# Performance work log

Hardware: AMD Instinct MI355X
Metric: run time of the kernel (lower is better)

Reference implementation:

```python
import jax, jax.numpy as jnp
import numpy as np

N_GRID = 262144   # grid vertices (all local, empty halo)
N_MESH = 40962    # icosahedral mesh level-6 vertices
N_EDGES = 524288  # mesh2grid bipartite edges
H = 128           # cfg.model.hidden_dim
LN_EPS = 1e-5


def layer_norm(x, g, b):
    m = jnp.mean(x, axis=-1, keepdims=True)
    v = jnp.var(x, axis=-1, keepdims=True)
    return (x - m) * jax.lax.rsqrt(v + LN_EPS) * g + b


def setup_inputs() -> dict:
    key = jax.random.key(0)
    ks = jax.random.split(key, 12)
    def w(k, shape, fan_in):
        return jax.random.normal(k, shape, jnp.float32) * (fan_in ** -0.5)
    return {
        "mesh2grid_edge_features": jax.random.normal(ks[0], (N_EDGES, H), jnp.float32),
        "grid_node_features": jax.random.normal(ks[1], (N_GRID, H), jnp.float32),
        "mesh_node_features": jax.random.normal(ks[2], (N_MESH, H), jnp.float32),
        # edge MLP: Linear(3H->H) -> SiLU -> Linear(H->H) -> LayerNorm, residual
        "edge_W1": w(ks[3], (3 * H, H), 3 * H), "edge_b1": jnp.zeros((H,), jnp.float32),
        "edge_W2": w(ks[4], (H, H), H), "edge_b2": jnp.zeros((H,), jnp.float32),
        "edge_ln_g": jnp.ones((H,), jnp.float32), "edge_ln_b": jnp.zeros((H,), jnp.float32),
        # node MLP: Linear(2H->H) -> SiLU -> Linear(H->H) -> LayerNorm
        "node_W1": w(ks[5], (2 * H, H), 2 * H), "node_b1": jnp.zeros((H,), jnp.float32),
        "node_W2": w(ks[6], (H, H), H), "node_b2": jnp.zeros((H,), jnp.float32),
        "node_ln_g": jnp.ones((H,), jnp.float32), "node_ln_b": jnp.zeros((H,), jnp.float32),
        "src_indices": jax.random.randint(ks[7], (N_EDGES,), 0, N_MESH, jnp.int32),
        "dst_indices": jax.random.randint(ks[8], (N_EDGES,), 0, N_GRID, jnp.int32),
    }


def reference(mesh2grid_edge_features, grid_node_features, mesh_node_features,
              edge_W1, edge_b1, edge_W2, edge_b2, edge_ln_g, edge_ln_b,
              node_W1, node_b1, node_W2, node_b2, node_ln_g, node_ln_b,
              src_indices, dst_indices):
    # --- edge block: gather src (mesh) / dst (grid), MLP, LN, residual ---
    src = mesh_node_features[src_indices]        # [E, H]  (augmented mesh == mesh, empty halo)
    dst = grid_node_features[dst_indices]        # [E, H]
    xe = jnp.concatenate([src, dst, mesh2grid_edge_features], axis=-1)  # [E, 3H]
    he = (jax.nn.silu(xe @ edge_W1 + edge_b1)) @ edge_W2 + edge_b2
    e_feats = mesh2grid_edge_features + layer_norm(he, edge_ln_g, edge_ln_b)  # [E, H]
    # --- node block: scatter-sum edges to grid nodes, MLP, LN ---
    agg = jax.ops.segment_sum(e_feats, dst_indices, num_segments=N_GRID)  # [N_grid, H]
    xn = jnp.concatenate([grid_node_features, agg], axis=-1)              # [N_grid, 2H]
    hn = (jax.nn.silu(xn @ node_W1 + node_b1)) @ node_W2 + node_b2
    n_feats = layer_norm(hn, node_ln_g, node_ln_b)
    return grid_node_features + n_feats
```

## Files before the change

kernel.cpp:

```cpp
#include <hip/hip_runtime.h>
#include <stdint.h>

#define HDIM 128
#define NGRID 262144
#define NMESH 40962
#define NEDGE 524288

typedef __attribute__((ext_vector_type(8))) short short8;
typedef __attribute__((ext_vector_type(4))) float f32x4;

__device__ __forceinline__ unsigned short f2bf(float f) {
  union { float f; uint32_t u; } v; v.f = f;
  uint32_t u = v.u;
  u += 0x7fffu + ((u >> 16) & 1u);
  return (unsigned short)(u >> 16);
}
__device__ __forceinline__ float bf2f(unsigned short h) {
  union { uint32_t u; float f; } v; v.u = ((uint32_t)h) << 16;
  return v.f;
}
__device__ __forceinline__ short8 cvt8(float4 a, float4 b) {
  short8 r;
  r[0] = (short)f2bf(a.x); r[1] = (short)f2bf(a.y);
  r[2] = (short)f2bf(a.z); r[3] = (short)f2bf(a.w);
  r[4] = (short)f2bf(b.x); r[5] = (short)f2bf(b.y);
  r[6] = (short)f2bf(b.z); r[7] = (short)f2bf(b.w);
  return r;
}

__global__ void pack_weights(const float* __restrict__ eW1, const float* __restrict__ eW2,
                             const float* __restrict__ nW1, const float* __restrict__ nW2,
                             unsigned short* __restrict__ ws)
{
  int i = blockIdx.x * 256 + threadIdx.x;
  unsigned short* eW1T = ws;
  unsigned short* eW2T = ws + 49152;
  unsigned short* nW1T = ws + 65536;
  unsigned short* nW2T = ws + 98304;
  if (i < 49152) {
    int c = i / 384, k = i % 384;
    eW1T[i] = f2bf(eW1[(size_t)k * 128 + c]);
  } else if (i < 65536) {
    int j = i - 49152; int c = j / 128, k = j % 128;
    eW2T[j] = f2bf(eW2[(size_t)k * 128 + c]);
  } else if (i < 98304) {
    int j = i - 65536; int c = j / 256, k = j % 256;
    nW1T[j] = f2bf(nW1[(size_t)k * 128 + c]);
  } else if (i < 114688) {
    int j = i - 98304; int c = j / 128, k = j % 128;
    nW2T[j] = f2bf(nW2[(size_t)k * 128 + c]);
  }
}

__global__ __launch_bounds__(256, 4)
void edge_kernel(const float* __restrict__ ef, const float* __restrict__ gridf,
                 const float* __restrict__ mesh,
                 const unsigned short* __restrict__ W1T, const unsigned short* __restrict__ W2T,
                 const float* __restrict__ b1, const float* __restrict__ b2,
                 const float* __restrict__ lng, const float* __restrict__ lnb,
                 const int* __restrict__ src, const int* __restrict__ dst,
                 float* __restrict__ agg)
{
  __shared__ __align__(16) unsigned short h1s[64][136];

  const int tid  = threadIdx.x;
  const int wave = tid >> 6;
  const int lane = tid & 63;
  const int l16  = lane & 15;
  const int g4   = lane >> 4;
  const int e0   = blockIdx.x * 64;
  const int arow = wave * 16 + l16;

  const int myS = src[e0 + arow];
  const int myD = dst[e0 + arow];
  const float* rowS = mesh  + (size_t)myS * HDIM;
  const float* rowD = gridf + (size_t)myD * HDIM;
  const float* rowE = ef    + (size_t)(e0 + arow) * HDIM;

  f32x4 acc[8];
  #pragma unroll
  for (int c = 0; c < 8; ++c) acc[c] = (f32x4){0.f, 0.f, 0.f, 0.f};

  const unsigned short* wl1 = W1T + (size_t)l16 * 384 + g4 * 8;

  #pragma unroll
  for (int part = 0; part < 3; ++part) {
    const float* base = (part == 0) ? rowS : (part == 1) ? rowD : rowE;
    #pragma unroll
    for (int kk = 0; kk < 4; ++kk) {
      const int ks = part * 4 + kk;
      const float* ap = base + kk * 32 + g4 * 8;
      float4 f0 = *reinterpret_cast<const float4*>(ap);
      float4 f1 = *reinterpret_cast<const float4*>(ap + 4);
      short8 a = cvt8(f0, f1);
      #pragma unroll
      for (int c = 0; c < 8; ++c) {
        short8 b = *reinterpret_cast<const short8*>(wl1 + (size_t)c * 16 * 384 + ks * 32);
        acc[c] = __builtin_amdgcn_mfma_f32_16x16x32_bf16(a, b, acc[c], 0, 0, 0);
      }
    }
  }

  #pragma unroll
  for (int c = 0; c < 8; ++c) {
    const int col = c * 16 + l16;
    float bb = b1[col];
    #pragma unroll
    for (int r = 0; r < 4; ++r) {
      float x = acc[c][r] + bb;
      float s = x / (1.f + __expf(-x));
      unsigned int h = f2bf(s);
      unsigned int other = __shfl_xor((int)h, 1);
      unsigned int packed = (l16 & 1) ? ((h << 16) | other) : ((other << 16) | h);
      if ((l16 & 1) == (r & 1)) {
        *reinterpret_cast<unsigned int*>(&h1s[wave * 16 + g4 * 4 + r][c * 16 + (l16 & ~1)]) = packed;
      }
    }
  }
  __syncthreads();

  f32x4 acc2[8];
  #pragma unroll
  for (int c = 0; c < 8; ++c) acc2[c] = (f32x4){0.f, 0.f, 0.f, 0.f};

  const unsigned short* wl2 = W2T + (size_t)l16 * 128 + g4 * 8;
  #pragma unroll
  for (int ks = 0; ks < 4; ++ks) {
    short8 a = *reinterpret_cast<const short8*>(&h1s[arow][ks * 32 + g4 * 8]);
    #pragma unroll
    for (int c = 0; c < 8; ++c) {
      short8 b = *reinterpret_cast<const short8*>(wl2 + (size_t)c * 16 * 128 + ks * 32);
      acc2[c] = __builtin_amdgcn_mfma_f32_16x16x32_bf16(a, b, acc2[c], 0, 0, 0);
    }
  }

  float vs[4] = {0.f, 0.f, 0.f, 0.f};
  float vq[4] = {0.f, 0.f, 0.f, 0.f};
  #pragma unroll
  for (int c = 0; c < 8; ++c) {
    float bb = b2[c * 16 + l16];
    #pragma unroll
    for (int r = 0; r < 4; ++r) {
      float x = acc2[c][r] + bb;
      acc2[c][r] = x;
      vs[r] += x;
      vq[r] += x * x;
    }
  }
  #pragma unroll
  for (int m = 1; m < 16; m <<= 1) {
    #pragma unroll
    for (int r = 0; r < 4; ++r) {
      vs[r] += __shfl_xor(vs[r], m);
      vq[r] += __shfl_xor(vq[r], m);
    }
  }
  float mean[4], rstd[4];
  #pragma unroll
  for (int r = 0; r < 4; ++r) {
    mean[r] = vs[r] * (1.f / 128.f);
    float var = vq[r] * (1.f / 128.f) - mean[r] * mean[r];
    rstd[r] = rsqrtf(var + 1e-5f);
  }
  int drow[4];
  #pragma unroll
  for (int r = 0; r < 4; ++r) drow[r] = dst[e0 + wave * 16 + g4 * 4 + r];

  #pragma unroll
  for (int c = 0; c < 8; ++c) {
    const int col = c * 16 + l16;
    float gg = lng[col], bb = lnb[col];
    #pragma unroll
    for (int r = 0; r < 4; ++r) {
      const int row = wave * 16 + g4 * 4 + r;
      float y = (acc2[c][r] - mean[r]) * rstd[r] * gg + bb;
      float e = ef[(size_t)(e0 + row) * HDIM + col] + y;
      unsafeAtomicAdd(&agg[(size_t)drow[r] * HDIM + col], e);
    }
  }
}

__global__ __launch_bounds__(256, 4)
void node_kernel(const float* __restrict__ gridf,
                 const unsigned short* __restrict__ W1T, const unsigned short* __restrict__ W2T,
                 const float* __restrict__ b1, const float* __restrict__ b2,
                 const float* __restrict__ lng, const float* __restrict__ lnb,
                 float* __restrict__ out)
{
  __shared__ __align__(16) unsigned short h1s[64][136];

  const int tid  = threadIdx.x;
  const int wave = tid >> 6;
  const int lane = tid & 63;
  const int l16  = lane & 15;
  const int g4   = lane >> 4;
  const int n0   = blockIdx.x * 64;
  const int arow = wave * 16 + l16;

  const float* rowG = gridf + (size_t)(n0 + arow) * HDIM;
  const float* rowA = out   + (size_t)(n0 + arow) * HDIM;

  f32x4 acc[8];
  #pragma unroll
  for (int c = 0; c < 8; ++c) acc[c] = (f32x4){0.f, 0.f, 0.f, 0.f};

  const unsigned short* wl1 = W1T + (size_t)l16 * 256 + g4 * 8;

  #pragma unroll
  for (int part = 0; part < 2; ++part) {
    const float* base = (part == 0) ? rowG : rowA;
    #pragma unroll
    for (int kk = 0; kk < 4; ++kk) {
      const int ks = part * 4 + kk;
      const float* ap = base + kk * 32 + g4 * 8;
      float4 f0 = *reinterpret_cast<const float4*>(ap);
      float4 f1 = *reinterpret_cast<const float4*>(ap + 4);
      short8 a = cvt8(f0, f1);
      #pragma unroll
      for (int c = 0; c < 8; ++c) {
        short8 b = *reinterpret_cast<const short8*>(wl1 + (size_t)c * 16 * 256 + ks * 32);
        acc[c] = __builtin_amdgcn_mfma_f32_16x16x32_bf16(a, b, acc[c], 0, 0, 0);
      }
    }
  }

  #pragma unroll
  for (int c = 0; c < 8; ++c) {
    const int col = c * 16 + l16;
    float bb = b1[col];
    #pragma unroll
    for (int r = 0; r < 4; ++r) {
      float x = acc[c][r] + bb;
      float s = x / (1.f + __expf(-x));
      unsigned int h = f2bf(s);
      unsigned int other = __shfl_xor((int)h, 1);
      unsigned int packed = (l16 & 1) ? ((h << 16) | other) : ((other << 16) | h);
      if ((l16 & 1) == (r & 1)) {
        *reinterpret_cast<unsigned int*>(&h1s[wave * 16 + g4 * 4 + r][c * 16 + (l16 & ~1)]) = packed;
      }
    }
  }
  __syncthreads();

  f32x4 acc2[8];
  #pragma unroll
  for (int c = 0; c < 8; ++c) acc2[c] = (f32x4){0.f, 0.f, 0.f, 0.f};

  const unsigned short* wl2 = W2T + (size_t)l16 * 128 + g4 * 8;
  #pragma unroll
  for (int ks = 0; ks < 4; ++ks) {
    short8 a = *reinterpret_cast<const short8*>(&h1s[arow][ks * 32 + g4 * 8]);
    #pragma unroll
    for (int c = 0; c < 8; ++c) {
      short8 b = *reinterpret_cast<const short8*>(wl2 + (size_t)c * 16 * 128 + ks * 32);
      acc2[c] = __builtin_amdgcn_mfma_f32_16x16x32_bf16(a, b, acc2[c], 0, 0, 0);
    }
  }

  float vs[4] = {0.f, 0.f, 0.f, 0.f};
  float vq[4] = {0.f, 0.f, 0.f, 0.f};
  #pragma unroll
  for (int c = 0; c < 8; ++c) {
    float bb = b2[c * 16 + l16];
    #pragma unroll
    for (int r = 0; r < 4; ++r) {
      float x = acc2[c][r] + bb;
      acc2[c][r] = x;
      vs[r] += x;
      vq[r] += x * x;
    }
  }
  #pragma unroll
  for (int m = 1; m < 16; m <<= 1) {
    #pragma unroll
    for (int r = 0; r < 4; ++r) {
      vs[r] += __shfl_xor(vs[r], m);
      vq[r] += __shfl_xor(vq[r], m);
    }
  }
  float mean[4], rstd[4];
  #pragma unroll
  for (int r = 0; r < 4; ++r) {
    mean[r] = vs[r] * (1.f / 128.f);
    float var = vq[r] * (1.f / 128.f) - mean[r] * mean[r];
    rstd[r] = rsqrtf(var + 1e-5f);
  }
  #pragma unroll
  for (int c = 0; c < 8; ++c) {
    const int col = c * 16 + l16;
    float gg = lng[col], bb = lnb[col];
    #pragma unroll
    for (int r = 0; r < 4; ++r) {
      const int row = wave * 16 + g4 * 4 + r;
      size_t idx = (size_t)(n0 + row) * HDIM + col;
      float y = (acc2[c][r] - mean[r]) * rstd[r] * gg + bb;
      out[idx] = gridf[idx] + y;
    }
  }
}

extern "C" void kernel_launch(void* const* d_in, const int* in_sizes, int n_in,
                              void* d_out, int out_size, void* d_ws, size_t ws_size,
                              hipStream_t stream)
{
  (void)in_sizes; (void)n_in; (void)out_size; (void)ws_size;
  const float* ef   = (const float*)d_in[0];
  const float* grid = (const float*)d_in[1];
  const float* mesh = (const float*)d_in[2];
  const float* eW1  = (const float*)d_in[3];
  const float* eb1  = (const float*)d_in[4];
  const float* eW2  = (const float*)d_in[5];
  const float* eb2  = (const float*)d_in[6];
  const float* elng = (const float*)d_in[7];
  const float* elnb = (const float*)d_in[8];
  const float* nW1  = (const float*)d_in[9];
  const float* nb1  = (const float*)d_in[10];
  const float* nW2  = (const float*)d_in[11];
  const float* nb2  = (const float*)d_in[12];
  const float* nlng = (const float*)d_in[13];
  const float* nlnb = (const float*)d_in[14];
  const int* src    = (const int*)d_in[15];
  const int* dst    = (const int*)d_in[16];
  float* out = (float*)d_out;
  unsigned short* ws = (unsigned short*)d_ws;

  hipMemsetAsync(out, 0, (size_t)NGRID * HDIM * sizeof(float), stream);
  pack_weights<<<448, 256, 0, stream>>>(eW1, eW2, nW1, nW2, ws);
  edge_kernel<<<NEDGE / 64, 256, 0, stream>>>(ef, grid, mesh,
      ws, ws + 49152, eb1, eb2, elng, elnb, src, dst, out);
  node_kernel<<<NGRID / 64, 256, 0, stream>>>(grid,
      ws + 65536, ws + 98304, nb1, nb2, nlng, nlnb, out);
}
```

Baseline: 957.4 us.

## Sort edges by destination and fuse edge and node MLPs per grid tile

Builds a CSR of edges grouped by destination grid node using a histogram, a three-pass scan and a scatter. A single fused kernel then processes 32 grid nodes per block: it gathers their edges, runs the edge MLP with 32x32x16 MFMAs, accumulates into LDS with shared atomics, and runs the node MLP directly. This removes the global float atomics and the round trip of the aggregate through HBM, and swaps the MFMA shape and the weight fragment layout. In exchange it adds several small preprocessing launches, global atomics in the histogram and scatter, and uneven per-block work because the number of edges per node varies.

```diff
diff --git a/kernel.cpp b/kernel.cpp
--- a/kernel.cpp
+++ b/kernel.cpp
@@ -7,295 +7,287 @@
 #define NEDGE 524288
 
 typedef __attribute__((ext_vector_type(8))) short short8;
-typedef __attribute__((ext_vector_type(4))) float f32x4;
-
-__device__ __forceinline__ unsigned short f2bf(float f) {
-  union { float f; uint32_t u; } v; v.f = f;
-  uint32_t u = v.u;
+typedef __attribute__((ext_vector_type(16))) float f32x16;
+typedef unsigned int u32;
+typedef unsigned long long u64;
+
+#define WS_COUNT   0x000000u
+#define WS_ROWPTR  0x100000u
+#define WS_WLOC    0x200010u
+#define WS_BSUM    0x300100u
+#define WS_SORTED  0x310000u
+#define WS_WEIGHTS 0x800000u
+#define WE1 0u
+#define WE2 49152u
+#define WN1 65536u
+#define WN2 98304u
+
+static __device__ __forceinline__ u32 f2bf_u(float f) {
+  union { float f; u32 u; } v; v.f = f;
+  u32 u = v.u;
   u += 0x7fffu + ((u >> 16) & 1u);
-  return (unsigned short)(u >> 16);
-}
-__device__ __forceinline__ float bf2f(unsigned short h) {
-  union { uint32_t u; float f; } v; v.u = ((uint32_t)h) << 16;
-  return v.f;
-}
-__device__ __forceinline__ short8 cvt8(float4 a, float4 b) {
+  return u >> 16;
+}
+static __device__ __forceinline__ unsigned short f2bf(float f) { return (unsigned short)f2bf_u(f); }
+static __device__ __forceinline__ u32 pack2bf(float a, float b) {
+  return f2bf_u(a) | (f2bf_u(b) << 16);
+}
+static __device__ __forceinline__ short8 cvt8(const float* p) {
+  float4 f0 = *(const float4*)p;
+  float4 f1 = *(const float4*)(p + 4);
   short8 r;
-  r[0] = (short)f2bf(a.x); r[1] = (short)f2bf(a.y);
-  r[2] = (short)f2bf(a.z); r[3] = (short)f2bf(a.w);
-  r[4] = (short)f2bf(b.x); r[5] = (short)f2bf(b.y);
-  r[6] = (short)f2bf(b.z); r[7] = (short)f2bf(b.w);
+  r[0] = (short)f2bf_u(f0.x); r[1] = (short)f2bf_u(f0.y);
+  r[2] = (short)f2bf_u(f0.z); r[3] = (short)f2bf_u(f0.w);
+  r[4] = (short)f2bf_u(f1.x); r[5] = (short)f2bf_u(f1.y);
+  r[6] = (short)f2bf_u(f1.z); r[7] = (short)f2bf_u(f1.w);
   return r;
 }
 
 __global__ void pack_weights(const float* __restrict__ eW1, const float* __restrict__ eW2,
                              const float* __restrict__ nW1, const float* __restrict__ nW2,
-                             unsigned short* __restrict__ ws)
+                             unsigned short* __restrict__ wp)
 {
   int i = blockIdx.x * 256 + threadIdx.x;
-  unsigned short* eW1T = ws;
-  unsigned short* eW2T = ws + 49152;
-  unsigned short* nW1T = ws + 65536;
-  unsigned short* nW2T = ws + 98304;
-  if (i < 49152) {
-    int c = i / 384, k = i % 384;
-    eW1T[i] = f2bf(eW1[(size_t)k * 128 + c]);
-  } else if (i < 65536) {
-    int j = i - 49152; int c = j / 128, k = j % 128;
-    eW2T[j] = f2bf(eW2[(size_t)k * 128 + c]);
-  } else if (i < 98304) {
-    int j = i - 65536; int c = j / 256, k = j % 256;
-    nW1T[j] = f2bf(nW1[(size_t)k * 128 + c]);
-  } else if (i < 114688) {
-    int j = i - 98304; int c = j / 128, k = j % 128;
-    nW2T[j] = f2bf(nW2[(size_t)k * 128 + c]);
-  }
-}
-
-__global__ __launch_bounds__(256, 4)
-void edge_kernel(const float* __restrict__ ef, const float* __restrict__ gridf,
-                 const float* __restrict__ mesh,
-                 const unsigned short* __restrict__ W1T, const unsigned short* __restrict__ W2T,
-                 const float* __restrict__ b1, const float* __restrict__ b2,
-                 const float* __restrict__ lng, const float* __restrict__ lnb,
-                 const int* __restrict__ src, const int* __restrict__ dst,
-                 float* __restrict__ agg)
+  const float* W; int KS; u32 base; int j;
+  if (i < 49152)       { W = eW1; KS = 24; base = WE1; j = i; }
+  else if (i < 65536)  { W = eW2; KS = 8;  base = WE2; j = i - 49152; }
+  else if (i < 98304)  { W = nW1; KS = 16; base = WN1; j = i - 65536; }
+  else if (i < 114688) { W = nW2; KS = 8;  base = WN2; j = i - 98304; }
+  else return;
+  int ii = j & 7, l = (j >> 3) & 63, frag = j >> 9;
+  int ks = frag % KS, w = frag / KS;
+  int row = w * 32 + (l & 31);
+  int k = ks * 16 + (l >> 5) * 8 + ii;
+  wp[base + j] = f2bf(W[(size_t)k * 128 + row]);
+}
+
+__global__ void hist_k(const int* __restrict__ dst, u32* __restrict__ cnt) {
+  int e = blockIdx.x * 256 + threadIdx.x;
+  atomicAdd(&cnt[dst[e]], 1u);
+}
+
+__global__ void scan1(const u32* __restrict__ cnt, u32* __restrict__ rp, u32* __restrict__ bsum) {
+  int t = threadIdx.x, b = blockIdx.x;
+  int i0 = b * 1024 + t * 4;
+  uint4 v = *(const uint4*)(cnt + i0);
+  u32 s = v.x + v.y + v.z + v.w;
+  u32 sc = s;
+  #pragma unroll
+  for (int d = 1; d < 64; d <<= 1) {
+    u32 n = (u32)__shfl_up((int)sc, d);
+    if ((t & 63) >= d) sc += n;
+  }
+  __shared__ u32 wsum[4];
+  if ((t & 63) == 63) wsum[t >> 6] = sc;
+  __syncthreads();
+  u32 woff = 0;
+  for (int w = 0; w < (t >> 6); ++w) woff += wsum[w];
+  u32 ex = woff + sc - s;
+  rp[i0] = ex; rp[i0 + 1] = ex + v.x; rp[i0 + 2] = ex + v.x + v.y; rp[i0 + 3] = ex + v.x + v.y + v.z;
+  if (t == 255) bsum[b] = woff + sc;
+}
+
+__global__ void scan2(u32* __restrict__ bsum) {
+  int t = threadIdx.x;
+  u32 s = bsum[t];
+  u32 sc = s;
+  #pragma unroll
+  for (int d = 1; d < 64; d <<= 1) {
+    u32 n = (u32)__shfl_up((int)sc, d);
+    if ((t & 63) >= d) sc += n;
+  }
+  __shared__ u32 wsum[4];
+  if ((t & 63) == 63) wsum[t >> 6] = sc;
+  __syncthreads();
+  u32 woff = 0;
+  for (int w = 0; w < (t >> 6); ++w) woff += wsum[w];
+  bsum[t] = woff + sc - s;
+}
+
+__global__ void scan3(u32* __restrict__ rp, u32* __restrict__ wloc, const u32* __restrict__ bsum) {
+  int t = threadIdx.x, b = blockIdx.x;
+  int i0 = b * 1024 + t * 4;
+  u32 off = bsum[b];
+  #pragma unroll
+  for (int j = 0; j < 4; ++j) { u32 vv = rp[i0 + j] + off; rp[i0 + j] = vv; wloc[i0 + j] = vv; }
+  if (b == 0 && t == 0) rp[NGRID] = NEDGE;
+}
+
+__global__ void scatter_k(const int* __restrict__ src, const int* __restrict__ dst,
+                          u32* __restrict__ wloc, u64* __restrict__ sorted) {
+  int e = blockIdx.x * 256 + threadIdx.x;
+  int d = dst[e];
+  u32 pos = atomicAdd(&wloc[d], 1u);
+  sorted[pos] = (u64)(u32)src[e] | ((u64)(u32)d << 16) | ((u64)(u32)e << 34);
+}
+
+__global__ __launch_bounds__(256, 3)
+void fused_kernel(const float* __restrict__ ef, const float* __restrict__ gridf,
+                  const float* __restrict__ mesh,
+                  const unsigned short* __restrict__ wp,
+                  const float* __restrict__ eb1, const float* __restrict__ eb2,
+                  const float* __restrict__ elng, const float* __restrict__ elnb,
+                  const float* __restrict__ nb1, const float* __restrict__ nb2,
+                  const float* __restrict__ nlng, const float* __restrict__ nlnb,
+                  const u32* __restrict__ rowptr, const u64* __restrict__ sorted,
+                  float* __restrict__ out)
 {
-  __shared__ __align__(16) unsigned short h1s[64][136];
-
-  const int tid  = threadIdx.x;
-  const int wave = tid >> 6;
-  const int lane = tid & 63;
-  const int l16  = lane & 15;
-  const int g4   = lane >> 4;
-  const int e0   = blockIdx.x * 64;
-  const int arow = wave * 16 + l16;
-
-  const int myS = src[e0 + arow];
-  const int myD = dst[e0 + arow];
-  const float* rowS = mesh  + (size_t)myS * HDIM;
-  const float* rowD = gridf + (size_t)myD * HDIM;
-  const float* rowE = ef    + (size_t)(e0 + arow) * HDIM;
-
-  f32x4 acc[8];
-  #pragma unroll
-  for (int c = 0; c < 8; ++c) acc[c] = (f32x4){0.f, 0.f, 0.f, 0.f};
-
-  const unsigned short* wl1 = W1T + (size_t)l16 * 384 + g4 * 8;
-
-  #pragma unroll
-  for (int part = 0; part < 3; ++part) {
-    const float* base = (part == 0) ? rowS : (part == 1) ? rowD : rowE;
-    #pragma unroll
-    for (int kk = 0; kk < 4; ++kk) {
-      const int ks = part * 4 + kk;
-      const float* ap = base + kk * 32 + g4 * 8;
-      float4 f0 = *reinterpret_cast<const float4*>(ap);
-      float4 f1 = *reinterpret_cast<const float4*>(ap + 4);
-      short8 a = cvt8(f0, f1);
+  __shared__ unsigned short xeLDS[32 * 384];
+  __shared__ unsigned short h1LDS[32 * 128];
+  __shared__ float aggLDS[32 * 129];
+  __shared__ float statsLDS[4][32][2];
+  __shared__ u32 srE[32], dlE[32], oeE[32];
+
+  const int tid = threadIdx.x;
+  const int wv = tid >> 6, ln = tid & 63, l31 = ln & 63 & 31, hi = ln >> 5;
+  const int n0 = blockIdx.x * 32;
+  const int rs = (int)rowptr[n0], re = (int)rowptr[n0 + 32];
+  const int swzE = (l31 & 15) << 3;
+
+  for (int i = tid; i < 32 * 129; i += 256) aggLDS[i] = 0.f;
+  __syncthreads();
+
+  const short8* w1p = (const short8*)(wp + WE1) + wv * 24 * 64 + ln;
+  const short8* w2p = (const short8*)(wp + WE2) + wv * 8 * 64 + ln;
+
+  for (int base = rs; base < re; base += 32) {
+    if (tid < 32) {
+      int p = base + tid; if (p >= re) p = re - 1;
+      u64 v = sorted[p];
+      srE[tid] = (u32)(v & 0xffffu);
+      dlE[tid] = (u32)((v >> 16) & 0x3ffffu) - (u32)n0;
+      oeE[tid] = (u32)(v >> 34);
+    }
+    __syncthreads();
+    for (int j = tid; j < 32 * 48; j += 256) {
+      int e = j / 48, u = j - e * 48;
+      int col0 = u * 8;
+      const float* bp;
+      if (col0 < 128)      bp = mesh  + (size_t)srE[e] * HDIM + col0;
+      else if (col0 < 256) bp = gridf + (size_t)(n0 + dlE[e]) * HDIM + (col0 - 128);
+      else                 bp = ef    + (size_t)oeE[e] * HDIM + (col0 - 256);
+      short8 v = cvt8(bp);
+      *(short8*)(xeLDS + e * 384 + (col0 ^ ((e & 15) << 3))) = v;
+    }
+    __syncthreads();
+
+    f32x16 acc1 = (f32x16)(0.f);
+    #pragma unroll 8
+    for (int ks = 0; ks < 24; ++ks) {
+      short8 A = w1p[ks * 64];
+      short8 B = *(const short8*)(xeLDS + l31 * 384 + ((ks * 16 + hi * 8) ^ swzE));
+      acc1 = __builtin_amdgcn_mfma_f32_32x32x16_bf16(A, B, acc1, 0, 0, 0);
+    }
+    #pragma unroll
+    for (int q = 0; q < 4; ++q) {
       #pragma unroll
-      for (int c = 0; c < 8; ++c) {
-        short8 b = *reinterpret_cast<const short8*>(wl1 + (size_t)c * 16 * 384 + ks * 32);
-        acc[c] = __builtin_amdgcn_mfma_f32_16x16x32_bf16(a, b, acc[c], 0, 0, 0);
+      for (int m = 0; m < 2; ++m) {
+        int r0 = q * 4 + m * 2;
+        int col = 32 * wv + 8 * q + 4 * hi + 2 * m;
+        float2 bb = *(const float2*)(eb1 + col);
+        float x0 = acc1[r0] + bb.x, x1 = acc1[r0 + 1] + bb.y;
+        x0 = x0 / (1.f + __expf(-x0));
+        x1 = x1 / (1.f + __expf(-x1));
+        *(u32*)(h1LDS + (l31 * 128 + (col ^ swzE))) = pack2bf(x0, x1);
       }
     }
-  }
-
-  #pragma unroll
-  for (int c = 0; c < 8; ++c) {
-    const int col = c * 16 + l16;
-    float bb = b1[col];
-    #pragma unroll
-    for (int r = 0; r < 4; ++r) {
-      float x = acc[c][r] + bb;
-      float s = x / (1.f + __expf(-x));
-      unsigned int h = f2bf(s);
-      unsigned int other = __shfl_xor((int)h, 1);
-      unsigned int packed = (l16 & 1) ? ((h << 16) | other) : ((other << 16) | h);
-      if ((l16 & 1) == (r & 1)) {
-        *reinterpret_cast<unsigned int*>(&h1s[wave * 16 + g4 * 4 + r][c * 16 + (l16 & ~1)]) = packed;
-      }
-    }
-  }
-  __syncthreads();
-
-  f32x4 acc2[8];
-  #pragma unroll
-  for (int c = 0; c < 8; ++c) acc2[c] = (f32x4){0.f, 0.f, 0.f, 0.f};
-
-  const unsigned short* wl2 = W2T + (size_t)l16 * 128 + g4 * 8;
-  #pragma unroll
-  for (int ks = 0; ks < 4; ++ks) {
-    short8 a = *reinterpret_cast<const short8*>(&h1s[arow][ks * 32 + g4 * 8]);
-    #pragma unroll
-    for (int c = 0; c < 8; ++c) {
-      short8 b = *reinterpret_cast<const short8*>(wl2 + (size_t)c * 16 * 128 + ks * 32);
-      acc2[c] = __builtin_amdgcn_mfma_f32_16x16x32_bf16(a, b, acc2[c], 0, 0, 0);
-    }
-  }
-
-  float vs[4] = {0.f, 0.f, 0.f, 0.f};
-  float vq[4] = {0.f, 0.f, 0.f, 0.f};
-  #pragma unroll
-  for (int c = 0; c < 8; ++c) {
-    float bb = b2[c * 16 + l16];
-    #pragma unroll
-    for (int r = 0; r < 4; ++r) {
-      float x = acc2[c][r] + bb;
-      acc2[c][r] = x;
-      vs[r] += x;
-      vq[r] += x * x;
-    }
-  }
-  #pragma unroll
-  for (int m = 1; m < 16; m <<= 1) {
-    #pragma unroll
-    for (int r = 0; r < 4; ++r) {
-      vs[r] += __shfl_xor(vs[r], m);
-      vq[r] += __shfl_xor(vq[r], m);
-    }
-  }
-  float mean[4], rstd[4];
-  #pragma unroll
-  for (int r = 0; r < 4; ++r) {
-    mean[r] = vs[r] * (1.f / 128.f);
-    float var = vq[r] * (1.f / 128.f) - mean[r] * mean[r];
-    rstd[r] = rsqrtf(var + 1e-5f);
-  }
-  int drow[4];
-  #pragma unroll
-  for (int r = 0; r < 4; ++r) drow[r] = dst[e0 + wave * 16 + g4 * 4 + r];
-
-  #pragma unroll
-  for (int c = 0; c < 8; ++c) {
-    const int col = c * 16 + l16;
-    float gg = lng[col], bb = lnb[col];
-    #pragma unroll
-    for (int r = 0; r < 4; ++r) {
-      const int row = wave * 16 + g4 * 4 + r;
-      float y = (acc2[c][r] - mean[r]) * rstd[r] * gg + bb;
-      float e = ef[(size_t)(e0 + row) * HDIM + col] + y;
-      unsafeAtomicAdd(&agg[(size_t)drow[r] * HDIM + col], e);
-    }
-  }
-}
-
-__global__ __launch_bounds__(256, 4)
-void node_kernel(const float* __restrict__ gridf,
-                 const unsigned short* __restrict__ W1T, const unsigned short* __restrict__ W2T,
-                 const float* __restrict__ b1, const float* __restrict__ b2,
-                 const float* __restrict__ lng, const float* __restrict__ lnb,
-                 float* __restrict__ out)
-{
-  __shared__ __align__(16) unsigned short h1s[64][136];
-
-  const int tid  = threadIdx.x;
-  const int wave = tid >> 6;
-  const int lane = tid & 63;
-  const int l16  = lane & 15;
-  const int g4   = lane >> 4;
-  const int n0   = blockIdx.x * 64;
-  const int arow = wave * 16 + l16;
-
-  const float* rowG = gridf + (size_t)(n0 + arow) * HDIM;
-  const float* rowA = out   + (size_t)(n0 + arow) * HDIM;
-
-  f32x4 acc[8];
-  #pragma unroll
-  for (int c = 0; c < 8; ++c) acc[c] = (f32x4){0.f, 0.f, 0.f, 0.f};
-
-  const unsigned short* wl1 = W1T + (size_t)l16 * 256 + g4 * 8;
-
-  #pragma unroll
-  for (int part = 0; part < 2; ++part) {
-    const float* base = (part == 0) ? rowG : rowA;
-    #pragma unroll
-    for (int kk = 0; kk < 4; ++kk) {
-      const int ks = part * 4 + kk;
-      const float* ap = base + kk * 32 + g4 * 8;
-      float4 f0 = *reinterpret_cast<const float4*>(ap);
-      float4 f1 = *reinterpret_cast<const float4*>(ap + 4);
-      short8 a = cvt8(f0, f1);
+    __syncthreads();
+
+    f32x16 acc2 = (f32x16)(0.f);
+    #pragma unroll
+    for (int ks = 0; ks < 8; ++ks) {
+      short8 A = w2p[ks * 64];
+      short8 B = *(const short8*)(h1LDS + l31 * 128 + ((ks * 16 + hi * 8) ^ swzE));
+      acc2 = __builtin_amdgcn_mfma_f32_32x32x16_bf16(A, B, acc2, 0, 0, 0);
+    }
+    float vs = 0.f, vq = 0.f;
+    #pragma unroll
+    for (int r = 0; r < 16; ++r) {
+      int col = 32 * wv + (r & 3) + 8 * (r >> 2) + 4 * hi;
+      float x = acc2[r] + eb2[col];
+      acc2[r] = x; vs += x; vq += x * x;
+    }
+    vs += __shfl_xor(vs, 32); vq += __shfl_xor(vq, 32);
+    if (ln < 32) { statsLDS[wv][l31][0] = vs; statsLDS[wv][l31][1] = vq; }
+    __syncthreads();
+    float vsT = 0.f, vqT = 0.f;
+    #pragma unroll
+    for (int w2 = 0; w2 < 4; ++w2) { vsT += statsLDS[w2][l31][0]; vqT += statsLDS[w2][l31][1]; }
+    float mean = vsT * (1.f / 128.f);
+    float rstd = rsqrtf(vqT * (1.f / 128.f) - mean * mean + 1e-5f);
+    bool valid = (base + l31) < re;
+    int dl = (int)dlE[l31];
+    u32 oe = oeE[l31];
+    #pragma unroll
+    for (int r = 0; r < 16; ++r) {
+      int col = 32 * wv + (r & 3) + 8 * (r >> 2) + 4 * hi;
+      float val = (acc2[r] - mean) * rstd * elng[col] + elnb[col] + ef[(size_t)oe * HDIM + col];
+      if (valid) atomicAdd(&aggLDS[dl * 129 + col], val);
+    }
+    __syncthreads();
+  }
+
+  const short8* nw1p = (const short8*)(wp + WN1) + wv * 16 * 64 + ln;
+  const short8* nw2p = (const short8*)(wp + WN2) + wv * 8 * 64 + ln;
+
+  f32x16 acc1 = (f32x16)(0.f);
+  #pragma unroll 8
+  for (int ks = 0; ks < 16; ++ks) {
+    short8 A = nw1p[ks * 64];
+    short8 B;
+    if (ks < 8) {
+      B = cvt8(gridf + (size_t)(n0 + l31) * HDIM + ks * 16 + hi * 8);
+    } else {
+      const float* ap = aggLDS + l31 * 129 + (ks - 8) * 16 + hi * 8;
+      short8 t;
       #pragma unroll
-      for (int c = 0; c < 8; ++c) {
-        short8 b = *reinterpret_cast<const short8*>(wl1 + (size_t)c * 16 * 256 + ks * 32);
-        acc[c] = __builtin_amdgcn_mfma_f32_16x16x32_bf16(a, b, acc[c], 0, 0, 0);
-      }
-    }
-  }
-
-  #pragma unroll
-  for (int c = 0; c < 8; ++c) {
-    const int col = c * 16 + l16;
-    float bb = b1[col];
-    #pragma unroll
-    for (int r = 0; r < 4; ++r) {
-      float x = acc[c][r] + bb;
-      float s = x / (1.f + __expf(-x));
-      unsigned int h = f2bf(s);
-      unsigned int other = __shfl_xor((int)h, 1);
-      unsigned int packed = (l16 & 1) ? ((h << 16) | other) : ((other << 16) | h);
-      if ((l16 & 1) == (r & 1)) {
-        *reinterpret_cast<unsigned int*>(&h1s[wave * 16 + g4 * 4 + r][c * 16 + (l16 & ~1)]) = packed;
-      }
-    }
-  }
-  __syncthreads();
-
-  f32x4 acc2[8];
-  #pragma unroll
-  for (int c = 0; c < 8; ++c) acc2[c] = (f32x4){0.f, 0.f, 0.f, 0.f};
-
-  const unsigned short* wl2 = W2T + (size_t)l16 * 128 + g4 * 8;
-  #pragma unroll
-  for (int ks = 0; ks < 4; ++ks) {
-    short8 a = *reinterpret_cast<const short8*>(&h1s[arow][ks * 32 + g4 * 8]);
-    #pragma unroll
-    for (int c = 0; c < 8; ++c) {
-      short8 b = *reinterpret_cast<const short8*>(wl2 + (size_t)c * 16 * 128 + ks * 32);
-      acc2[c] = __builtin_amdgcn_mfma_f32_16x16x32_bf16(a, b, acc2[c], 0, 0, 0);
-    }
-  }
-
-  float vs[4] = {0.f, 0.f, 0.f, 0.f};
-  float vq[4] = {0.f, 0.f, 0.f, 0.f};
-  #pragma unroll
-  for (int c = 0; c < 8; ++c) {
-    float bb = b2[c * 16 + l16];
-    #pragma unroll
-    for (int r = 0; r < 4; ++r) {
-      float x = acc2[c][r] + bb;
-      acc2[c][r] = x;
-      vs[r] += x;
-      vq[r] += x * x;
-    }
-  }
-  #pragma unroll
-  for (int m = 1; m < 16; m <<= 1) {
-    #pragma unroll
-    for (int r = 0; r < 4; ++r) {
-      vs[r] += __shfl_xor(vs[r], m);
-      vq[r] += __shfl_xor(vq[r], m);
-    }
-  }
-  float mean[4], rstd[4];
-  #pragma unroll
-  for (int r = 0; r < 4; ++r) {
-    mean[r] = vs[r] * (1.f / 128.f);
-    float var = vq[r] * (1.f / 128.f) - mean[r] * mean[r];
-    rstd[r] = rsqrtf(var + 1e-5f);
-  }
-  #pragma unroll
-  for (int c = 0; c < 8; ++c) {
-    const int col = c * 16 + l16;
-    float gg = lng[col], bb = lnb[col];
-    #pragma unroll
-    for (int r = 0; r < 4; ++r) {
-      const int row = wave * 16 + g4 * 4 + r;
-      size_t idx = (size_t)(n0 + row) * HDIM + col;
-      float y = (acc2[c][r] - mean[r]) * rstd[r] * gg + bb;
-      out[idx] = gridf[idx] + y;
-    }
+      for (int i = 0; i < 8; ++i) t[i] = (short)f2bf_u(ap[i]);
+      B = t;
+    }
+    acc1 = __builtin_amdgcn_mfma_f32_32x32x16_bf16(A, B, acc1, 0, 0, 0);
+  }
+  #pragma unroll
+  for (int q = 0; q < 4; ++q) {
+    #pragma unroll
+    for (int m = 0; m < 2; ++m) {
+      int r0 = q * 4 + m * 2;
+      int col = 32 * wv + 8 * q + 4 * hi + 2 * m;
+      float2 bb = *(const float2*)(nb1 + col);
+      float x0 = acc1[r0] + bb.x, x1 = acc1[r0 + 1] + bb.y;
+      x0 = x0 / (1.f + __expf(-x0));
+      x1 = x1 / (1.f + __expf(-x1));
+      *(u32*)(h1LDS + (l31 * 128 + (col ^ swzE))) = pack2bf(x0, x1);
+    }
+  }
+  __syncthreads();
+
+  f32x16 acc2 = (f32x16)(0.f);
+  #pragma unroll
+  for (int ks = 0; ks < 8; ++ks) {
+    short8 A = nw2p[ks * 64];
+    short8 B = *(const short8*)(h1LDS + l31 * 128 + ((ks * 16 + hi * 8) ^ swzE));
+    acc2 = __builtin_amdgcn_mfma_f32_32x32x16_bf16(A, B, acc2, 0, 0, 0);
+  }
+  float vs = 0.f, vq = 0.f;
+  #pragma unroll
+  for (int r = 0; r < 16; ++r) {
+    int col = 32 * wv + (r & 3) + 8 * (r >> 2) + 4 * hi;
+    float x = acc2[r] + nb2[col];
+    acc2[r] = x; vs += x; vq += x * x;
+  }
+  vs += __shfl_xor(vs, 32); vq += __shfl_xor(vq, 32);
+  if (ln < 32) { statsLDS[wv][l31][0] = vs; statsLDS[wv][l31][1] = vq; }
+  __syncthreads();
+  float vsT = 0.f, vqT = 0.f;
+  #pragma unroll
+  for (int w2 = 0; w2 < 4; ++w2) { vsT += statsLDS[w2][l31][0]; vqT += statsLDS[w2][l31][1]; }
+  float mean = vsT * (1.f / 128.f);
+  float rstd = rsqrtf(vqT * (1.f / 128.f) - mean * mean + 1e-5f);
+  #pragma unroll
+  for (int r = 0; r < 16; ++r) {
+    int col = 32 * wv + (r & 3) + 8 * (r >> 2) + 4 * hi;
+    size_t idx = (size_t)(n0 + l31) * HDIM + col;
+    out[idx] = (acc2[r] - mean) * rstd * nlng[col] + nlnb[col] + gridf[idx];
   }
 }
 
@@ -322,12 +314,22 @@
   const int* src    = (const int*)d_in[15];
   const int* dst    = (const int*)d_in[16];
   float* out = (float*)d_out;
-  unsigned short* ws = (unsigned short*)d_ws;
-
-  hipMemsetAsync(out, 0, (size_t)NGRID * HDIM * sizeof(float), stream);
-  pack_weights<<<448, 256, 0, stream>>>(eW1, eW2, nW1, nW2, ws);
-  edge_kernel<<<NEDGE / 64, 256, 0, stream>>>(ef, grid, mesh,
-      ws, ws + 49152, eb1, eb2, elng, elnb, src, dst, out);
-  node_kernel<<<NGRID / 64, 256, 0, stream>>>(grid,
-      ws + 65536, ws + 98304, nb1, nb2, nlng, nlnb, out);
-}
+
+  unsigned char* wsb = (unsigned char*)d_ws;
+  u32* cnt  = (u32*)(wsb + WS_COUNT);
+  u32* rp   = (u32*)(wsb + WS_ROWPTR);
+  u32* wloc = (u32*)(wsb + WS_WLOC);
+  u32* bsum = (u32*)(wsb + WS_BSUM);
+  u64* sorted = (u64*)(wsb + WS_SORTED);
+  unsigned short* wp = (unsigned short*)(wsb + WS_WEIGHTS);
+
+  hipMemsetAsync(cnt, 0, (size_t)NGRID * 4, stream);
+  pack_weights<<<448, 256, 0, stream>>>(eW1, eW2, nW1, nW2, wp);
+  hist_k<<<NEDGE / 256, 256, 0, stream>>>(dst, cnt);
+  scan1<<<256, 256, 0, stream>>>(cnt, rp, bsum);
+  scan2<<<1, 256, 0, stream>>>(bsum);
+  scan3<<<256, 256, 0, stream>>>(rp, wloc, bsum);
+  scatter_k<<<NEDGE / 256, 256, 0, stream>>>(src, dst, wloc, sorted);
+  fused_kernel<<<NGRID / 32, 256, 0, stream>>>(ef, grid, mesh, wp,
+      eb1, eb2, elng, elnb, nb1, nb2, nlng, nlnb, rp, sorted, out);
+}
```

Result: faster. 859.8 us (-10.2%).
